# Performance work log

Hardware: AMD Instinct MI355X
Metric: run time of the kernel (lower is better)

The kernel has to match this reference:

```python
import jax, jax.numpy as jnp
import numpy as np

T = 1024
V = 512
K_BINS = jnp.array([1, 2, 3, 4, 5, 6, 7, 8, 12, 16, 24, 32, 48, 64, 96, 128], dtype=jnp.int32)
SPLIT_T = T // 2                      # int(T * 0.5)
CW = max(4, T // 20)                  # crossfade width = 51
FADE_START = SPLIT_T - CW // 2        # 487
FADE_END = SPLIT_T + CW // 2          # 537


def _early_weight():
    t = jnp.arange(T, dtype=jnp.float32)
    fade = 1.0 - (t - FADE_START) / (FADE_END - FADE_START)
    ew = jnp.where(t < FADE_START, 1.0, jnp.where(t < FADE_END, fade, 0.0))
    return ew.reshape(1, T, 1)


def setup_inputs() -> dict:
    key = jax.random.key(0)
    k = jax.random.split(key, 5)
    B = 64
    return {
        "x": jax.random.normal(k[0], (B, T, V), dtype=jnp.float32),
        "g_early_real": jax.random.normal(k[1], (V, 16), dtype=jnp.float32) * 0.1,
        "g_early_imag": jax.random.normal(k[2], (V, 16), dtype=jnp.float32) * 0.1,
        "g_late_real": jax.random.normal(k[3], (V, 16), dtype=jnp.float32) * 0.1,
        "g_late_imag": jax.random.normal(k[4], (V, 16), dtype=jnp.float32) * 0.1,
    }


def reference(x, g_early_real, g_early_imag, g_late_real, g_late_imag):
    # x: [B, T, V] real. rfft along time.
    X = jnp.fft.rfft(x, n=T, axis=1)              # [B, F, V] complex, F = T//2+1
    xb = X[:, K_BINS, :]                          # [B, K, V]
    # complex gain (1 + gr + i*gi), broadcast [1, K, V]
    g_e = (g_early_real + 1j * g_early_imag).T[None, :, :]
    g_l = (g_late_real + 1j * g_late_imag).T[None, :, :]
    Y_e = X.at[:, K_BINS, :].set(xb * (1.0 + g_e))
    Y_l = X.at[:, K_BINS, :].set(xb * (1.0 + g_l))
    y_early = jnp.fft.irfft(Y_e, n=T, axis=1)     # [B, T, V]
    y_late = jnp.fft.irfft(Y_l, n=T, axis=1)
    ew = _early_weight()
    return ew * y_early + (1.0 - ew) * y_late
```

## Files before the change

kernel.cpp:

```cpp
#include <hip/hip_runtime.h>
#include <math.h>

#define T_LEN 1024
#define VV 512
#define BB 64
#define NB 16
#define ANG_STEP 0.006135923151542565f
#define FADE_S 487
#define FADE_E 537

typedef float v2f __attribute__((ext_vector_type(2)));

__device__ constexpr int KB[NB] = {1,2,3,4,5,6,7,8,12,16,24,32,48,64,96,128};
__device__ constexpr float CWT[NB] = {
    0.9999811753f, 0.9999247018f, 0.9998305818f, 0.9996988187f,
    0.9995294175f, 0.9993223846f, 0.9990777278f, 0.9987954562f,
    0.9972904567f, 0.9951847267f, 0.9891765100f, 0.9807852804f,
    0.9569403357f, 0.9238795325f, 0.8314696123f, 0.7071067812f};
__device__ constexpr float SWT[NB] = {
    0.0061358846f, 0.0122715383f, 0.0184067299f, 0.0245412285f,
    0.0306748032f, 0.0368072229f, 0.0429382569f, 0.0490676743f,
    0.0735645636f, 0.0980171403f, 0.1467304745f, 0.1950903220f,
    0.2902846773f, 0.3826834324f, 0.5555702330f, 0.7071067812f};

__global__ __launch_bounds__(512) void k_fused(const float* __restrict__ x,
                                               const float* __restrict__ ger,
                                               const float* __restrict__ gei,
                                               const float* __restrict__ glr,
                                               const float* __restrict__ gli,
                                               float* __restrict__ Hg,
                                               float* __restrict__ out) {
    const int b    = blockIdx.x;
    const int vc   = blockIdx.y;
    const int tid  = threadIdx.x;
    const int wave = tid >> 6;
    const int lane = tid & 63;

    __shared__ __align__(16) float scr[4 * 128 * 8];

    const int trow = wave * 128;
    const int v0   = lane * 2;
    const float2* xrd = (const float2*)(x + ((size_t)b * T_LEN + trow) * VV + vc * 128) + lane;

    float ar0[NB], ai0[NB], ar1[NB], ai1[NB], c[NB], s[NB];
#pragma unroll
    for (int j = 0; j < NB; ++j) {
        ar0[j] = ai0[j] = ar1[j] = ai1[j] = 0.f;
        int n0 = (KB[j] * trow) & (T_LEN - 1);
        sincosf(ANG_STEP * (float)n0, &s[j], &c[j]);
    }

#define DFT_STEP(AV)                                            \
    do {                                                        \
        _Pragma("unroll")                                       \
        for (int j = 0; j < NB; ++j) {                          \
            ar0[j] = fmaf((AV).x, c[j], ar0[j]);                \
            ai0[j] = fmaf(-(AV).x, s[j], ai0[j]);               \
            ar1[j] = fmaf((AV).y, c[j], ar1[j]);                \
            ai1[j] = fmaf(-(AV).y, s[j], ai1[j]);               \
            float cn = fmaf(c[j], CWT[j], -(s[j] * SWT[j]));    \
            float sn = fmaf(s[j], CWT[j], c[j] * SWT[j]);       \
            c[j] = cn; s[j] = sn;                               \
        }                                                       \
    } while (0)

    {
        float2 a0 = xrd[(size_t)0 * 256];
        float2 a1 = xrd[(size_t)1 * 256];
        float2 a2 = xrd[(size_t)2 * 256];
        float2 a3 = xrd[(size_t)3 * 256];
#pragma unroll 1
        for (int i = 0; i < 124; i += 4) {
            float2 b0 = xrd[(size_t)(i + 4) * 256];
            float2 b1 = xrd[(size_t)(i + 5) * 256];
            float2 b2 = xrd[(size_t)(i + 6) * 256];
            float2 b3 = xrd[(size_t)(i + 7) * 256];
            DFT_STEP(a0); DFT_STEP(a1); DFT_STEP(a2); DFT_STEP(a3);
            a0 = b0; a1 = b1; a2 = b2; a3 = b3;
        }
        DFT_STEP(a0); DFT_STEP(a1); DFT_STEP(a2); DFT_STEP(a3);
    }
#undef DFT_STEP

    float Xre_lo[2], Xre_hi[2], Xim_lo[2], Xim_hi[2];

#define RED_ROUND(SRC0, SRC1, JOFF, DST)                                   \
    do {                                                                   \
        if (wave < 4) {                                                    \
            _Pragma("unroll")                                              \
            for (int jj = 0; jj < 8; ++jj) {                               \
                scr[((size_t)wave * 128 + v0)     * 8 + jj] = SRC0[(JOFF) + jj]; \
                scr[((size_t)wave * 128 + v0 + 1) * 8 + jj] = SRC1[(JOFF) + jj]; \
            }                                                              \
        }                                                                  \
        __syncthreads();                                                   \
        if (wave >= 4) {                                                   \
            const int w2 = wave - 4;                                       \
            _Pragma("unroll")                                              \
            for (int jj = 0; jj < 8; ++jj) {                               \
                scr[((size_t)w2 * 128 + v0)     * 8 + jj] += SRC0[(JOFF) + jj]; \
                scr[((size_t)w2 * 128 + v0 + 1) * 8 + jj] += SRC1[(JOFF) + jj]; \
            }                                                              \
        }                                                                  \
        __syncthreads();                                                   \
        _Pragma("unroll")                                                  \
        for (int q = 0; q < 2; ++q) {                                      \
            const int cc = tid * 2 + q;                                    \
            const int vq = cc >> 3, jq = cc & 7;                           \
            DST[q] = scr[((size_t)0 * 128 + vq) * 8 + jq]                  \
                   + scr[((size_t)1 * 128 + vq) * 8 + jq]                  \
                   + scr[((size_t)2 * 128 + vq) * 8 + jq]                  \
                   + scr[((size_t)3 * 128 + vq) * 8 + jq];                 \
        }                                                                  \
        __syncthreads();                                                   \
    } while (0)

    RED_ROUND(ar0, ar1, 0, Xre_lo);
    RED_ROUND(ar0, ar1, 8, Xre_hi);
    RED_ROUND(ai0, ai1, 0, Xim_lo);
    RED_ROUND(ai0, ai1, 8, Xim_hi);
#undef RED_ROUND

    const float scale = 2.0f / (float)T_LEN;
    {
        float* hg = Hg + (size_t)b * 64 * VV;
#pragma unroll
        for (int q = 0; q < 2; ++q) {
            const int cc = tid * 2 + q;
            const int vq = cc >> 3;
            const int vg = vc * 128 + vq;
#pragma unroll
            for (int half = 0; half < 2; ++half) {
                const int jq = (cc & 7) + half * 8;
                const float Xr = half ? Xre_hi[q] : Xre_lo[q];
                const float Xi = half ? Xim_hi[q] : Xim_lo[q];
                float er = ger[vg * NB + jq], ei = gei[vg * NB + jq];
                float lr = glr[vg * NB + jq], li = gli[vg * NB + jq];
                float here  = (Xr * er - Xi * ei) * scale;
                float heimN = -(Xr * ei + Xi * er) * scale;
                float hlre  = (Xr * lr - Xi * li) * scale;
                float hlimN = -(Xr * li + Xi * lr) * scale;
                hg[(size_t)jq * VV + vg]        = here;
                hg[(size_t)(16 + jq) * VV + vg] = heimN;
                hg[(size_t)(32 + jq) * VV + vg] = hlre;
                hg[(size_t)(48 + jq) * VV + vg] = hlimN;
            }
        }
    }
    __syncthreads();

    float hr0[NB], hi0[NB], hr1[NB], hi1[NB];
    {
        const int qb = (wave < 4) ? 0 : 32;
        const float* hgr = Hg + (size_t)b * 64 * VV + vc * 128;
#pragma unroll
        for (int j = 0; j < NB; ++j) {
            hr0[j] = hgr[(size_t)(qb + j) * VV + v0];
            hr1[j] = hgr[(size_t)(qb + j) * VV + v0 + 1];
            hi0[j] = hgr[(size_t)(qb + 16 + j) * VV + v0];
            hi1[j] = hgr[(size_t)(qb + 16 + j) * VV + v0 + 1];
        }
#pragma unroll
        for (int j = 0; j < NB; ++j) {
            int n0 = (KB[j] * trow) & (T_LEN - 1);
            sincosf(ANG_STEP * (float)n0, &s[j], &c[j]);
        }
    }

    v2f* ow = (v2f*)(out + ((size_t)b * T_LEN + trow) * VV + vc * 128) + lane;

#define APPLY_STEP(TT, AV)                                      \
    do {                                                        \
        float s0 = 0.f, s1 = 0.f;                               \
        _Pragma("unroll")                                       \
        for (int j = 0; j < NB; ++j) {                          \
            s0 = fmaf(hr0[j], c[j], s0);                        \
            s0 = fmaf(hi0[j], s[j], s0);                        \
            s1 = fmaf(hr1[j], c[j], s1);                        \
            s1 = fmaf(hi1[j], s[j], s1);                        \
            float cn = fmaf(c[j], CWT[j], -(s[j] * SWT[j]));    \
            float sn = fmaf(s[j], CWT[j], c[j] * SWT[j]);       \
            c[j] = cn; s[j] = sn;                               \
        }                                                       \
        v2f ov; ov.x = (AV).x + s0; ov.y = (AV).y + s1;         \
        __builtin_nontemporal_store(ov, &ow[(size_t)(TT) * 256]); \
    } while (0)

    {
        float2 a0 = xrd[(size_t)0 * 256];
        float2 a1 = xrd[(size_t)1 * 256];
        float2 a2 = xrd[(size_t)2 * 256];
        float2 a3 = xrd[(size_t)3 * 256];
#pragma unroll 1
        for (int i = 0; i < 124; i += 4) {
            float2 b0 = xrd[(size_t)(i + 4) * 256];
            float2 b1 = xrd[(size_t)(i + 5) * 256];
            float2 b2 = xrd[(size_t)(i + 6) * 256];
            float2 b3 = xrd[(size_t)(i + 7) * 256];
            APPLY_STEP(i + 0, a0); APPLY_STEP(i + 1, a1);
            APPLY_STEP(i + 2, a2); APPLY_STEP(i + 3, a3);
            a0 = b0; a1 = b1; a2 = b2; a3 = b3;
        }
        APPLY_STEP(124, a0); APPLY_STEP(125, a1);
        APPLY_STEP(126, a2); APPLY_STEP(127, a3);
    }
#undef APPLY_STEP
}

__global__ __launch_bounds__(512) void k_fixup(const float* __restrict__ x,
                                               const float* __restrict__ H,
                                               float* __restrict__ out) {
    const int b   = blockIdx.x;
    const int tz  = blockIdx.y;
    const int tid = threadIdx.x;
    const int ts  = tz ? 512 : FADE_S;
    const int te  = tz ? FADE_E : 512;
    const int nt  = te - ts;

    __shared__ float2 tab[32][NB];
    for (int i = tid; i < nt * NB; i += 512) {
        int t = i >> 4, j = i & 15;
        int idx = (KB[j] * (ts + t)) & (T_LEN - 1);
        float ss, cc; sincosf(ANG_STEP * (float)idx, &ss, &cc);
        tab[t][j] = make_float2(cc, ss);
    }

    float er[NB], ei[NB], lr[NB], li[NB];
    const float* hp = H + (size_t)b * 64 * VV + tid;
#pragma unroll
    for (int j = 0; j < NB; ++j) {
        er[j] = hp[(size_t)j        * VV];
        ei[j] = hp[(size_t)(16 + j) * VV];
        lr[j] = hp[(size_t)(32 + j) * VV];
        li[j] = hp[(size_t)(48 + j) * VV];
    }
    __syncthreads();

    const float* xrd = x + ((size_t)b * T_LEN + ts) * VV + tid;
    float*       ow  = out + ((size_t)b * T_LEN + ts) * VV + tid;

    for (int t = 0; t < nt; ++t) {
        float av = xrd[(size_t)t * VV];
        const int tg = ts + t;
        float se = 0.f, sl = 0.f;
#pragma unroll
        for (int j = 0; j < NB; ++j) {
            float2 cs = tab[t][j];
            se = fmaf(er[j], cs.x, se); se = fmaf(ei[j], cs.y, se);
            sl = fmaf(lr[j], cs.x, sl); sl = fmaf(li[j], cs.y, sl);
        }
        float w = 1.0f - (float)(tg - FADE_S) * (1.0f / 50.0f);
        ow[(size_t)t * VV] = av + fmaf(w, se - sl, sl);
    }
}

extern "C" void kernel_launch(void* const* d_in, const int* in_sizes, int n_in,
                              void* d_out, int out_size, void* d_ws, size_t ws_size,
                              hipStream_t stream) {
    (void)in_sizes; (void)n_in; (void)out_size; (void)ws_size;
    const float* x   = (const float*)d_in[0];
    const float* ger = (const float*)d_in[1];
    const float* gei = (const float*)d_in[2];
    const float* glr = (const float*)d_in[3];
    const float* gli = (const float*)d_in[4];
    float* out = (float*)d_out;

    float* Hg = (float*)d_ws;

    k_fused<<<dim3(BB, 4), 512, 0, stream>>>(x, ger, gei, glr, gli, Hg, out);
    k_fixup<<<dim3(BB, 2), 512, 0, stream>>>(x, Hg, out);
}
```

Baseline: 126.2 us.

## Double block size to 1024 threads, halve time rows per wave, stage gains in LDS

New measurement: 193.3 us. 1.53x slower.

```diff
diff --git a/kernel.cpp b/kernel.cpp
--- a/kernel.cpp
+++ b/kernel.cpp
@@ -23,22 +23,23 @@
     0.0735645636f, 0.0980171403f, 0.1467304745f, 0.1950903220f,
     0.2902846773f, 0.3826834324f, 0.5555702330f, 0.7071067812f};
 
-__global__ __launch_bounds__(512) void k_fused(const float* __restrict__ x,
-                                               const float* __restrict__ ger,
-                                               const float* __restrict__ gei,
-                                               const float* __restrict__ glr,
-                                               const float* __restrict__ gli,
-                                               float* __restrict__ Hg,
-                                               float* __restrict__ out) {
+__global__ __launch_bounds__(1024) void k_fused(const float* __restrict__ x,
+                                                const float* __restrict__ ger,
+                                                const float* __restrict__ gei,
+                                                const float* __restrict__ glr,
+                                                const float* __restrict__ gli,
+                                                float* __restrict__ Hg,
+                                                float* __restrict__ out) {
     const int b    = blockIdx.x;
     const int vc   = blockIdx.y;
     const int tid  = threadIdx.x;
     const int wave = tid >> 6;
     const int lane = tid & 63;
 
-    __shared__ __align__(16) float scr[4 * 128 * 8];
-
-    const int trow = wave * 128;
+    __shared__ __align__(16) float scr[8 * 128 * 9];
+    __shared__ __align__(16) float HB[64 * 128];
+
+    const int trow = wave * 64;
     const int v0   = lane * 2;
     const float2* xrd = (const float2*)(x + ((size_t)b * T_LEN + trow) * VV + vc * 128) + lane;
 
@@ -70,7 +71,7 @@
         float2 a2 = xrd[(size_t)2 * 256];
         float2 a3 = xrd[(size_t)3 * 256];
 #pragma unroll 1
-        for (int i = 0; i < 124; i += 4) {
+        for (int i = 0; i < 60; i += 4) {
             float2 b0 = xrd[(size_t)(i + 4) * 256];
             float2 b1 = xrd[(size_t)(i + 5) * 256];
             float2 b2 = xrd[(size_t)(i + 6) * 256];
@@ -82,37 +83,37 @@
     }
 #undef DFT_STEP
 
-    float Xre_lo[2], Xre_hi[2], Xim_lo[2], Xim_hi[2];
-
-#define RED_ROUND(SRC0, SRC1, JOFF, DST)                                   \
-    do {                                                                   \
-        if (wave < 4) {                                                    \
-            _Pragma("unroll")                                              \
-            for (int jj = 0; jj < 8; ++jj) {                               \
-                scr[((size_t)wave * 128 + v0)     * 8 + jj] = SRC0[(JOFF) + jj]; \
-                scr[((size_t)wave * 128 + v0 + 1) * 8 + jj] = SRC1[(JOFF) + jj]; \
-            }                                                              \
-        }                                                                  \
-        __syncthreads();                                                   \
-        if (wave >= 4) {                                                   \
-            const int w2 = wave - 4;                                       \
-            _Pragma("unroll")                                              \
-            for (int jj = 0; jj < 8; ++jj) {                               \
-                scr[((size_t)w2 * 128 + v0)     * 8 + jj] += SRC0[(JOFF) + jj]; \
-                scr[((size_t)w2 * 128 + v0 + 1) * 8 + jj] += SRC1[(JOFF) + jj]; \
-            }                                                              \
-        }                                                                  \
-        __syncthreads();                                                   \
-        _Pragma("unroll")                                                  \
-        for (int q = 0; q < 2; ++q) {                                      \
-            const int cc = tid * 2 + q;                                    \
-            const int vq = cc >> 3, jq = cc & 7;                           \
-            DST[q] = scr[((size_t)0 * 128 + vq) * 8 + jq]                  \
-                   + scr[((size_t)1 * 128 + vq) * 8 + jq]                  \
-                   + scr[((size_t)2 * 128 + vq) * 8 + jq]                  \
-                   + scr[((size_t)3 * 128 + vq) * 8 + jq];                 \
-        }                                                                  \
-        __syncthreads();                                                   \
+    float Xre_lo, Xre_hi, Xim_lo, Xim_hi;
+    const int vq = tid >> 3;
+    const int jq = tid & 7;
+
+#define RED_ROUND(SRC0, SRC1, JOFF, DST)                                         \
+    do {                                                                         \
+        if (wave < 8) {                                                          \
+            _Pragma("unroll")                                                    \
+            for (int jj = 0; jj < 8; ++jj) {                                     \
+                scr[((size_t)wave * 128 + v0)     * 9 + jj] = SRC0[(JOFF) + jj]; \
+                scr[((size_t)wave * 128 + v0 + 1) * 9 + jj] = SRC1[(JOFF) + jj]; \
+            }                                                                    \
+        }                                                                        \
+        __syncthreads();                                                         \
+        if (wave >= 8) {                                                         \
+            const int w2 = wave - 8;                                             \
+            _Pragma("unroll")                                                    \
+            for (int jj = 0; jj < 8; ++jj) {                                     \
+                scr[((size_t)w2 * 128 + v0)     * 9 + jj] += SRC0[(JOFF) + jj];  \
+                scr[((size_t)w2 * 128 + v0 + 1) * 9 + jj] += SRC1[(JOFF) + jj];  \
+            }                                                                    \
+        }                                                                        \
+        __syncthreads();                                                         \
+        {                                                                        \
+            float acc = 0.f;                                                     \
+            _Pragma("unroll")                                                    \
+            for (int w = 0; w < 8; ++w)                                          \
+                acc += scr[((size_t)w * 128 + vq) * 9 + jq];                     \
+            DST = acc;                                                           \
+        }                                                                        \
+        __syncthreads();                                                         \
     } while (0)
 
     RED_ROUND(ar0, ar1, 0, Xre_lo);
@@ -124,41 +125,39 @@
     const float scale = 2.0f / (float)T_LEN;
     {
         float* hg = Hg + (size_t)b * 64 * VV;
-#pragma unroll
-        for (int q = 0; q < 2; ++q) {
-            const int cc = tid * 2 + q;
-            const int vq = cc >> 3;
-            const int vg = vc * 128 + vq;
-#pragma unroll
-            for (int half = 0; half < 2; ++half) {
-                const int jq = (cc & 7) + half * 8;
-                const float Xr = half ? Xre_hi[q] : Xre_lo[q];
-                const float Xi = half ? Xim_hi[q] : Xim_lo[q];
-                float er = ger[vg * NB + jq], ei = gei[vg * NB + jq];
-                float lr = glr[vg * NB + jq], li = gli[vg * NB + jq];
-                float here  = (Xr * er - Xi * ei) * scale;
-                float heimN = -(Xr * ei + Xi * er) * scale;
-                float hlre  = (Xr * lr - Xi * li) * scale;
-                float hlimN = -(Xr * li + Xi * lr) * scale;
-                hg[(size_t)jq * VV + vg]        = here;
-                hg[(size_t)(16 + jq) * VV + vg] = heimN;
-                hg[(size_t)(32 + jq) * VV + vg] = hlre;
-                hg[(size_t)(48 + jq) * VV + vg] = hlimN;
-            }
+        const int vg = vc * 128 + vq;
+#pragma unroll
+        for (int half = 0; half < 2; ++half) {
+            const int jc = jq + half * 8;
+            const float Xr = half ? Xre_hi : Xre_lo;
+            const float Xi = half ? Xim_hi : Xim_lo;
+            float er = ger[vg * NB + jc], ei = gei[vg * NB + jc];
+            float lr = glr[vg * NB + jc], li = gli[vg * NB + jc];
+            float here  = (Xr * er - Xi * ei) * scale;
+            float heimN = -(Xr * ei + Xi * er) * scale;
+            float hlre  = (Xr * lr - Xi * li) * scale;
+            float hlimN = -(Xr * li + Xi * lr) * scale;
+            HB[jc * 128 + vq]        = here;
+            HB[(16 + jc) * 128 + vq] = heimN;
+            HB[(32 + jc) * 128 + vq] = hlre;
+            HB[(48 + jc) * 128 + vq] = hlimN;
+            hg[(size_t)jc * VV + vg]        = here;
+            hg[(size_t)(16 + jc) * VV + vg] = heimN;
+            hg[(size_t)(32 + jc) * VV + vg] = hlre;
+            hg[(size_t)(48 + jc) * VV + vg] = hlimN;
         }
     }
     __syncthreads();
 
     float hr0[NB], hi0[NB], hr1[NB], hi1[NB];
     {
-        const int qb = (wave < 4) ? 0 : 32;
-        const float* hgr = Hg + (size_t)b * 64 * VV + vc * 128;
+        const int qb = (wave < 8) ? 0 : 32;
 #pragma unroll
         for (int j = 0; j < NB; ++j) {
-            hr0[j] = hgr[(size_t)(qb + j) * VV + v0];
-            hr1[j] = hgr[(size_t)(qb + j) * VV + v0 + 1];
-            hi0[j] = hgr[(size_t)(qb + 16 + j) * VV + v0];
-            hi1[j] = hgr[(size_t)(qb + 16 + j) * VV + v0 + 1];
+            hr0[j] = HB[(qb + j) * 128 + v0];
+            hr1[j] = HB[(qb + j) * 128 + v0 + 1];
+            hi0[j] = HB[(qb + 16 + j) * 128 + v0];
+            hi1[j] = HB[(qb + 16 + j) * 128 + v0 + 1];
         }
 #pragma unroll
         for (int j = 0; j < NB; ++j) {
@@ -192,7 +191,7 @@
         float2 a2 = xrd[(size_t)2 * 256];
         float2 a3 = xrd[(size_t)3 * 256];
 #pragma unroll 1
-        for (int i = 0; i < 124; i += 4) {
+        for (int i = 0; i < 60; i += 4) {
             float2 b0 = xrd[(size_t)(i + 4) * 256];
             float2 b1 = xrd[(size_t)(i + 5) * 256];
             float2 b2 = xrd[(size_t)(i + 6) * 256];
@@ -201,8 +200,8 @@
             APPLY_STEP(i + 2, a2); APPLY_STEP(i + 3, a3);
             a0 = b0; a1 = b1; a2 = b2; a3 = b3;
         }
-        APPLY_STEP(124, a0); APPLY_STEP(125, a1);
-        APPLY_STEP(126, a2); APPLY_STEP(127, a3);
+        APPLY_STEP(60, a0); APPLY_STEP(61, a1);
+        APPLY_STEP(62, a2); APPLY_STEP(63, a3);
     }
 #undef APPLY_STEP
 }
@@ -267,6 +266,6 @@
 
     float* Hg = (float*)d_ws;
 
-    k_fused<<<dim3(BB, 4), 512, 0, stream>>>(x, ger, gei, glr, gli, Hg, out);
+    k_fused<<<dim3(BB, 4), 1024, 0, stream>>>(x, ger, gei, glr, gli, Hg, out);
     k_fixup<<<dim3(BB, 2), 512, 0, stream>>>(x, Hg, out);
 }
```

## Halve per-thread columns, doubling grid, and use Chebyshev twiddle recurrence

Applied to the files above, without the earlier changes.

Result: slower. 131.9 us (+4.5%).

```diff
diff --git a/kernel.cpp b/kernel.cpp
--- a/kernel.cpp
+++ b/kernel.cpp
@@ -8,8 +8,6 @@
 #define ANG_STEP 0.006135923151542565f
 #define FADE_S 487
 #define FADE_E 537
-
-typedef float v2f __attribute__((ext_vector_type(2)));
 
 __device__ constexpr int KB[NB] = {1,2,3,4,5,6,7,8,12,16,24,32,48,64,96,128};
 __device__ constexpr float CWT[NB] = {
@@ -22,6 +20,11 @@
     0.0306748032f, 0.0368072229f, 0.0429382569f, 0.0490676743f,
     0.0735645636f, 0.0980171403f, 0.1467304745f, 0.1950903220f,
     0.2902846773f, 0.3826834324f, 0.5555702330f, 0.7071067812f};
+__device__ constexpr float C2W[NB] = {
+    1.9999623506f, 1.9998494036f, 1.9996611636f, 1.9993976374f,
+    1.9990588350f, 1.9986447692f, 1.9981554556f, 1.9975909124f,
+    1.9945809134f, 1.9903694534f, 1.9783530200f, 1.9615705608f,
+    1.9138806714f, 1.8477590650f, 1.6629392246f, 1.4142135624f};
 
 __global__ __launch_bounds__(512) void k_fused(const float* __restrict__ x,
                                                const float* __restrict__ ger,
@@ -36,45 +39,45 @@
     const int wave = tid >> 6;
     const int lane = tid & 63;
 
-    __shared__ __align__(16) float scr[4 * 128 * 8];
+    __shared__ __align__(16) float scr[4 * 64 * 17];
+    __shared__ __align__(16) float HB[64 * 64];
 
     const int trow = wave * 128;
-    const int v0   = lane * 2;
-    const float2* xrd = (const float2*)(x + ((size_t)b * T_LEN + trow) * VV + vc * 128) + lane;
-
-    float ar0[NB], ai0[NB], ar1[NB], ai1[NB], c[NB], s[NB];
+    const float* xrd = x + ((size_t)b * T_LEN + trow) * VV + vc * 64 + lane;
+
+    float ar[NB], ai[NB], c[NB], s[NB], cp[NB], sp[NB];
 #pragma unroll
     for (int j = 0; j < NB; ++j) {
-        ar0[j] = ai0[j] = ar1[j] = ai1[j] = 0.f;
+        ar[j] = ai[j] = 0.f;
         int n0 = (KB[j] * trow) & (T_LEN - 1);
         sincosf(ANG_STEP * (float)n0, &s[j], &c[j]);
-    }
-
-#define DFT_STEP(AV)                                            \
-    do {                                                        \
-        _Pragma("unroll")                                       \
-        for (int j = 0; j < NB; ++j) {                          \
-            ar0[j] = fmaf((AV).x, c[j], ar0[j]);                \
-            ai0[j] = fmaf(-(AV).x, s[j], ai0[j]);               \
-            ar1[j] = fmaf((AV).y, c[j], ar1[j]);                \
-            ai1[j] = fmaf(-(AV).y, s[j], ai1[j]);               \
-            float cn = fmaf(c[j], CWT[j], -(s[j] * SWT[j]));    \
-            float sn = fmaf(s[j], CWT[j], c[j] * SWT[j]);       \
-            c[j] = cn; s[j] = sn;                               \
-        }                                                       \
+        cp[j] = fmaf(c[j], CWT[j], s[j] * SWT[j]);
+        sp[j] = fmaf(s[j], CWT[j], -(c[j] * SWT[j]));
+    }
+
+#define DFT_STEP(AV)                                           \
+    do {                                                       \
+        _Pragma("unroll")                                      \
+        for (int j = 0; j < NB; ++j) {                         \
+            ar[j] = fmaf((AV), c[j], ar[j]);                   \
+            ai[j] = fmaf(-(AV), s[j], ai[j]);                  \
+            float cn = fmaf(C2W[j], c[j], -cp[j]);             \
+            float sn = fmaf(C2W[j], s[j], -sp[j]);             \
+            cp[j] = c[j]; sp[j] = s[j]; c[j] = cn; s[j] = sn;  \
+        }                                                      \
     } while (0)
 
     {
-        float2 a0 = xrd[(size_t)0 * 256];
-        float2 a1 = xrd[(size_t)1 * 256];
-        float2 a2 = xrd[(size_t)2 * 256];
-        float2 a3 = xrd[(size_t)3 * 256];
+        float a0 = xrd[(size_t)0 * VV];
+        float a1 = xrd[(size_t)1 * VV];
+        float a2 = xrd[(size_t)2 * VV];
+        float a3 = xrd[(size_t)3 * VV];
 #pragma unroll 1
         for (int i = 0; i < 124; i += 4) {
-            float2 b0 = xrd[(size_t)(i + 4) * 256];
-            float2 b1 = xrd[(size_t)(i + 5) * 256];
-            float2 b2 = xrd[(size_t)(i + 6) * 256];
-            float2 b3 = xrd[(size_t)(i + 7) * 256];
+            float b0 = xrd[(size_t)(i + 4) * VV];
+            float b1 = xrd[(size_t)(i + 5) * VV];
+            float b2 = xrd[(size_t)(i + 6) * VV];
+            float b3 = xrd[(size_t)(i + 7) * VV];
             DFT_STEP(a0); DFT_STEP(a1); DFT_STEP(a2); DFT_STEP(a3);
             a0 = b0; a1 = b1; a2 = b2; a3 = b3;
         }
@@ -82,44 +85,54 @@
     }
 #undef DFT_STEP
 
-    float Xre_lo[2], Xre_hi[2], Xim_lo[2], Xim_hi[2];
-
-#define RED_ROUND(SRC0, SRC1, JOFF, DST)                                   \
-    do {                                                                   \
-        if (wave < 4) {                                                    \
-            _Pragma("unroll")                                              \
-            for (int jj = 0; jj < 8; ++jj) {                               \
-                scr[((size_t)wave * 128 + v0)     * 8 + jj] = SRC0[(JOFF) + jj]; \
-                scr[((size_t)wave * 128 + v0 + 1) * 8 + jj] = SRC1[(JOFF) + jj]; \
-            }                                                              \
-        }                                                                  \
-        __syncthreads();                                                   \
-        if (wave >= 4) {                                                   \
-            const int w2 = wave - 4;                                       \
-            _Pragma("unroll")                                              \
-            for (int jj = 0; jj < 8; ++jj) {                               \
-                scr[((size_t)w2 * 128 + v0)     * 8 + jj] += SRC0[(JOFF) + jj]; \
-                scr[((size_t)w2 * 128 + v0 + 1) * 8 + jj] += SRC1[(JOFF) + jj]; \
-            }                                                              \
-        }                                                                  \
-        __syncthreads();                                                   \
-        _Pragma("unroll")                                                  \
-        for (int q = 0; q < 2; ++q) {                                      \
-            const int cc = tid * 2 + q;                                    \
-            const int vq = cc >> 3, jq = cc & 7;                           \
-            DST[q] = scr[((size_t)0 * 128 + vq) * 8 + jq]                  \
-                   + scr[((size_t)1 * 128 + vq) * 8 + jq]                  \
-                   + scr[((size_t)2 * 128 + vq) * 8 + jq]                  \
-                   + scr[((size_t)3 * 128 + vq) * 8 + jq];                 \
-        }                                                                  \
-        __syncthreads();                                                   \
-    } while (0)
-
-    RED_ROUND(ar0, ar1, 0, Xre_lo);
-    RED_ROUND(ar0, ar1, 8, Xre_hi);
-    RED_ROUND(ai0, ai1, 0, Xim_lo);
-    RED_ROUND(ai0, ai1, 8, Xim_hi);
-#undef RED_ROUND
+    float Xre[2], Xim[2];
+
+    if (wave < 4) {
+#pragma unroll
+        for (int j = 0; j < NB; ++j)
+            scr[((size_t)wave * 64 + lane) * 17 + j] = ar[j];
+    }
+    __syncthreads();
+    if (wave >= 4) {
+        const int w2 = wave - 4;
+#pragma unroll
+        for (int j = 0; j < NB; ++j)
+            scr[((size_t)w2 * 64 + lane) * 17 + j] += ar[j];
+    }
+    __syncthreads();
+#pragma unroll
+    for (int q = 0; q < 2; ++q) {
+        const int cc = tid * 2 + q;
+        const int vq = cc >> 4, jq = cc & 15;
+        Xre[q] = scr[((size_t)0 * 64 + vq) * 17 + jq]
+               + scr[((size_t)1 * 64 + vq) * 17 + jq]
+               + scr[((size_t)2 * 64 + vq) * 17 + jq]
+               + scr[((size_t)3 * 64 + vq) * 17 + jq];
+    }
+    __syncthreads();
+
+    if (wave < 4) {
+#pragma unroll
+        for (int j = 0; j < NB; ++j)
+            scr[((size_t)wave * 64 + lane) * 17 + j] = ai[j];
+    }
+    __syncthreads();
+    if (wave >= 4) {
+        const int w2 = wave - 4;
+#pragma unroll
+        for (int j = 0; j < NB; ++j)
+            scr[((size_t)w2 * 64 + lane) * 17 + j] += ai[j];
+    }
+    __syncthreads();
+#pragma unroll
+    for (int q = 0; q < 2; ++q) {
+        const int cc = tid * 2 + q;
+        const int vq = cc >> 4, jq = cc & 15;
+        Xim[q] = scr[((size_t)0 * 64 + vq) * 17 + jq]
+               + scr[((size_t)1 * 64 + vq) * 17 + jq]
+               + scr[((size_t)2 * 64 + vq) * 17 + jq]
+               + scr[((size_t)3 * 64 + vq) * 17 + jq];
+    }
 
     const float scale = 2.0f / (float)T_LEN;
     {
@@ -127,76 +140,71 @@
 #pragma unroll
         for (int q = 0; q < 2; ++q) {
             const int cc = tid * 2 + q;
-            const int vq = cc >> 3;
-            const int vg = vc * 128 + vq;
-#pragma unroll
-            for (int half = 0; half < 2; ++half) {
-                const int jq = (cc & 7) + half * 8;
-                const float Xr = half ? Xre_hi[q] : Xre_lo[q];
-                const float Xi = half ? Xim_hi[q] : Xim_lo[q];
-                float er = ger[vg * NB + jq], ei = gei[vg * NB + jq];
-                float lr = glr[vg * NB + jq], li = gli[vg * NB + jq];
-                float here  = (Xr * er - Xi * ei) * scale;
-                float heimN = -(Xr * ei + Xi * er) * scale;
-                float hlre  = (Xr * lr - Xi * li) * scale;
-                float hlimN = -(Xr * li + Xi * lr) * scale;
-                hg[(size_t)jq * VV + vg]        = here;
-                hg[(size_t)(16 + jq) * VV + vg] = heimN;
-                hg[(size_t)(32 + jq) * VV + vg] = hlre;
-                hg[(size_t)(48 + jq) * VV + vg] = hlimN;
-            }
-        }
-    }
-    __syncthreads();
-
-    float hr0[NB], hi0[NB], hr1[NB], hi1[NB];
+            const int vq = cc >> 4, jq = cc & 15;
+            const int vg = vc * 64 + vq;
+            float er = ger[vg * NB + jq], ei = gei[vg * NB + jq];
+            float lr = glr[vg * NB + jq], li = gli[vg * NB + jq];
+            float here  = (Xre[q] * er - Xim[q] * ei) * scale;
+            float heimN = -(Xre[q] * ei + Xim[q] * er) * scale;
+            float hlre  = (Xre[q] * lr - Xim[q] * li) * scale;
+            float hlimN = -(Xre[q] * li + Xim[q] * lr) * scale;
+            HB[jq * 64 + vq]        = here;
+            HB[(16 + jq) * 64 + vq] = heimN;
+            HB[(32 + jq) * 64 + vq] = hlre;
+            HB[(48 + jq) * 64 + vq] = hlimN;
+            hg[(size_t)jq * VV + vg]        = here;
+            hg[(size_t)(16 + jq) * VV + vg] = heimN;
+            hg[(size_t)(32 + jq) * VV + vg] = hlre;
+            hg[(size_t)(48 + jq) * VV + vg] = hlimN;
+        }
+    }
+    __syncthreads();
+
+    float hr[NB], hi[NB];
     {
         const int qb = (wave < 4) ? 0 : 32;
-        const float* hgr = Hg + (size_t)b * 64 * VV + vc * 128;
 #pragma unroll
         for (int j = 0; j < NB; ++j) {
-            hr0[j] = hgr[(size_t)(qb + j) * VV + v0];
-            hr1[j] = hgr[(size_t)(qb + j) * VV + v0 + 1];
-            hi0[j] = hgr[(size_t)(qb + 16 + j) * VV + v0];
-            hi1[j] = hgr[(size_t)(qb + 16 + j) * VV + v0 + 1];
+            hr[j] = HB[(qb + j) * 64 + lane];
+            hi[j] = HB[(qb + 16 + j) * 64 + lane];
         }
 #pragma unroll
         for (int j = 0; j < NB; ++j) {
             int n0 = (KB[j] * trow) & (T_LEN - 1);
             sincosf(ANG_STEP * (float)n0, &s[j], &c[j]);
-        }
-    }
-
-    v2f* ow = (v2f*)(out + ((size_t)b * T_LEN + trow) * VV + vc * 128) + lane;
-
-#define APPLY_STEP(TT, AV)                                      \
-    do {                                                        \
-        float s0 = 0.f, s1 = 0.f;                               \
-        _Pragma("unroll")                                       \
-        for (int j = 0; j < NB; ++j) {                          \
-            s0 = fmaf(hr0[j], c[j], s0);                        \
-            s0 = fmaf(hi0[j], s[j], s0);                        \
-            s1 = fmaf(hr1[j], c[j], s1);                        \
-            s1 = fmaf(hi1[j], s[j], s1);                        \
-            float cn = fmaf(c[j], CWT[j], -(s[j] * SWT[j]));    \
-            float sn = fmaf(s[j], CWT[j], c[j] * SWT[j]);       \
-            c[j] = cn; s[j] = sn;                               \
-        }                                                       \
-        v2f ov; ov.x = (AV).x + s0; ov.y = (AV).y + s1;         \
-        __builtin_nontemporal_store(ov, &ow[(size_t)(TT) * 256]); \
+            cp[j] = fmaf(c[j], CWT[j], s[j] * SWT[j]);
+            sp[j] = fmaf(s[j], CWT[j], -(c[j] * SWT[j]));
+        }
+    }
+
+    float* ow = out + ((size_t)b * T_LEN + trow) * VV + vc * 64 + lane;
+
+#define APPLY_STEP(TT, AV)                                     \
+    do {                                                       \
+        float s0 = 0.f;                                        \
+        _Pragma("unroll")                                      \
+        for (int j = 0; j < NB; ++j) {                         \
+            s0 = fmaf(hr[j], c[j], s0);                        \
+            s0 = fmaf(hi[j], s[j], s0);                        \
+            float cn = fmaf(C2W[j], c[j], -cp[j]);             \
+            float sn = fmaf(C2W[j], s[j], -sp[j]);             \
+            cp[j] = c[j]; sp[j] = s[j]; c[j] = cn; s[j] = sn;  \
+        }                                                      \
+        __builtin_nontemporal_store((AV) + s0,                 \
+            &ow[(size_t)(TT) * VV]);                           \
     } while (0)
 
     {
-        float2 a0 = xrd[(size_t)0 * 256];
-        float2 a1 = xrd[(size_t)1 * 256];
-        float2 a2 = xrd[(size_t)2 * 256];
-        float2 a3 = xrd[(size_t)3 * 256];
+        float a0 = xrd[(size_t)0 * VV];
+        float a1 = xrd[(size_t)1 * VV];
+        float a2 = xrd[(size_t)2 * VV];
+        float a3 = xrd[(size_t)3 * VV];
 #pragma unroll 1
         for (int i = 0; i < 124; i += 4) {
-            float2 b0 = xrd[(size_t)(i + 4) * 256];
-            float2 b1 = xrd[(size_t)(i + 5) * 256];
-            float2 b2 = xrd[(size_t)(i + 6) * 256];
-            float2 b3 = xrd[(size_t)(i + 7) * 256];
+            float b0 = xrd[(size_t)(i + 4) * VV];
+            float b1 = xrd[(size_t)(i + 5) * VV];
+            float b2 = xrd[(size_t)(i + 6) * VV];
+            float b3 = xrd[(size_t)(i + 7) * VV];
             APPLY_STEP(i + 0, a0); APPLY_STEP(i + 1, a1);
             APPLY_STEP(i + 2, a2); APPLY_STEP(i + 3, a3);
             a0 = b0; a1 = b1; a2 = b2; a3 = b3;
@@ -267,6 +275,6 @@
 
     float* Hg = (float*)d_ws;
 
-    k_fused<<<dim3(BB, 4), 512, 0, stream>>>(x, ger, gei, glr, gli, Hg, out);
+    k_fused<<<dim3(BB, 8), 512, 0, stream>>>(x, ger, gei, glr, gli, Hg, out);
     k_fixup<<<dim3(BB, 2), 512, 0, stream>>>(x, Hg, out);
 }
```

## Split fused DFT/apply kernel into two kernels over time halves for more blocks

Applied to the files above, without the earlier changes.

New measurement: 129.0 us. 1.02x slower.

```diff
diff --git a/kernel.cpp b/kernel.cpp
--- a/kernel.cpp
+++ b/kernel.cpp
@@ -23,22 +23,18 @@
     0.0735645636f, 0.0980171403f, 0.1467304745f, 0.1950903220f,
     0.2902846773f, 0.3826834324f, 0.5555702330f, 0.7071067812f};
 
-__global__ __launch_bounds__(512) void k_fused(const float* __restrict__ x,
-                                               const float* __restrict__ ger,
-                                               const float* __restrict__ gei,
-                                               const float* __restrict__ glr,
-                                               const float* __restrict__ gli,
-                                               float* __restrict__ Hg,
-                                               float* __restrict__ out) {
+__global__ __launch_bounds__(512) void k_dft(const float* __restrict__ x,
+                                             float* __restrict__ Xpart) {
     const int b    = blockIdx.x;
     const int vc   = blockIdx.y;
+    const int th   = blockIdx.z;
     const int tid  = threadIdx.x;
     const int wave = tid >> 6;
     const int lane = tid & 63;
 
-    __shared__ __align__(16) float scr[4 * 128 * 8];
-
-    const int trow = wave * 128;
+    __shared__ __align__(16) float scr[4 * 128 * 17];
+
+    const int trow = th * 512 + wave * 64;
     const int v0   = lane * 2;
     const float2* xrd = (const float2*)(x + ((size_t)b * T_LEN + trow) * VV + vc * 128) + lane;
 
@@ -70,7 +66,7 @@
         float2 a2 = xrd[(size_t)2 * 256];
         float2 a3 = xrd[(size_t)3 * 256];
 #pragma unroll 1
-        for (int i = 0; i < 124; i += 4) {
+        for (int i = 0; i < 60; i += 4) {
             float2 b0 = xrd[(size_t)(i + 4) * 256];
             float2 b1 = xrd[(size_t)(i + 5) * 256];
             float2 b2 = xrd[(size_t)(i + 6) * 256];
@@ -82,91 +78,118 @@
     }
 #undef DFT_STEP
 
-    float Xre_lo[2], Xre_hi[2], Xim_lo[2], Xim_hi[2];
-
-#define RED_ROUND(SRC0, SRC1, JOFF, DST)                                   \
+    float Xre[4], Xim[4];
+
+#define RED_ROUND(SRC0, SRC1, DST)                                         \
     do {                                                                   \
         if (wave < 4) {                                                    \
             _Pragma("unroll")                                              \
-            for (int jj = 0; jj < 8; ++jj) {                               \
-                scr[((size_t)wave * 128 + v0)     * 8 + jj] = SRC0[(JOFF) + jj]; \
-                scr[((size_t)wave * 128 + v0 + 1) * 8 + jj] = SRC1[(JOFF) + jj]; \
+            for (int j = 0; j < NB; ++j) {                                 \
+                scr[((size_t)wave * 128 + v0)     * 17 + j] = SRC0[j];     \
+                scr[((size_t)wave * 128 + v0 + 1) * 17 + j] = SRC1[j];     \
             }                                                              \
         }                                                                  \
         __syncthreads();                                                   \
         if (wave >= 4) {                                                   \
             const int w2 = wave - 4;                                       \
             _Pragma("unroll")                                              \
-            for (int jj = 0; jj < 8; ++jj) {                               \
-                scr[((size_t)w2 * 128 + v0)     * 8 + jj] += SRC0[(JOFF) + jj]; \
-                scr[((size_t)w2 * 128 + v0 + 1) * 8 + jj] += SRC1[(JOFF) + jj]; \
+            for (int j = 0; j < NB; ++j) {                                 \
+                scr[((size_t)w2 * 128 + v0)     * 17 + j] += SRC0[j];      \
+                scr[((size_t)w2 * 128 + v0 + 1) * 17 + j] += SRC1[j];      \
             }                                                              \
         }                                                                  \
         __syncthreads();                                                   \
         _Pragma("unroll")                                                  \
-        for (int q = 0; q < 2; ++q) {                                      \
-            const int cc = tid * 2 + q;                                    \
-            const int vq = cc >> 3, jq = cc & 7;                           \
-            DST[q] = scr[((size_t)0 * 128 + vq) * 8 + jq]                  \
-                   + scr[((size_t)1 * 128 + vq) * 8 + jq]                  \
-                   + scr[((size_t)2 * 128 + vq) * 8 + jq]                  \
-                   + scr[((size_t)3 * 128 + vq) * 8 + jq];                 \
+        for (int q = 0; q < 4; ++q) {                                      \
+            const int cc = tid * 4 + q;                                    \
+            const int vq = cc >> 4, jq = cc & 15;                          \
+            DST[q] = scr[((size_t)0 * 128 + vq) * 17 + jq]                 \
+                   + scr[((size_t)1 * 128 + vq) * 17 + jq]                 \
+                   + scr[((size_t)2 * 128 + vq) * 17 + jq]                 \
+                   + scr[((size_t)3 * 128 + vq) * 17 + jq];                \
         }                                                                  \
         __syncthreads();                                                   \
     } while (0)
 
-    RED_ROUND(ar0, ar1, 0, Xre_lo);
-    RED_ROUND(ar0, ar1, 8, Xre_hi);
-    RED_ROUND(ai0, ai1, 0, Xim_lo);
-    RED_ROUND(ai0, ai1, 8, Xim_hi);
+    RED_ROUND(ar0, ar1, Xre);
+    RED_ROUND(ai0, ai1, Xim);
 #undef RED_ROUND
+
+    float* xp = Xpart + ((size_t)((b * 4 + vc) * 2 + th)) * 32 * 128;
+#pragma unroll
+    for (int q = 0; q < 4; ++q) {
+        const int cc = tid * 4 + q;
+        const int vq = cc >> 4, jq = cc & 15;
+        xp[(size_t)jq * 128 + vq]        = Xre[q];
+        xp[(size_t)(16 + jq) * 128 + vq] = Xim[q];
+    }
+}
+
+__global__ __launch_bounds__(512) void k_comb_apply(const float* __restrict__ x,
+                                                    const float* __restrict__ ger,
+                                                    const float* __restrict__ gei,
+                                                    const float* __restrict__ glr,
+                                                    const float* __restrict__ gli,
+                                                    const float* __restrict__ Xpart,
+                                                    float* __restrict__ Hg,
+                                                    float* __restrict__ out) {
+    const int b    = blockIdx.x;
+    const int vc   = blockIdx.y;
+    const int th   = blockIdx.z;
+    const int tid  = threadIdx.x;
+    const int wave = tid >> 6;
+    const int lane = tid & 63;
+
+    __shared__ __align__(16) float HB[64 * 128];
 
     const float scale = 2.0f / (float)T_LEN;
     {
+        const float* xp0 = Xpart + ((size_t)((b * 4 + vc) * 2 + 0)) * 32 * 128;
+        const float* xp1 = Xpart + ((size_t)((b * 4 + vc) * 2 + 1)) * 32 * 128;
         float* hg = Hg + (size_t)b * 64 * VV;
 #pragma unroll
-        for (int q = 0; q < 2; ++q) {
-            const int cc = tid * 2 + q;
-            const int vq = cc >> 3;
-            const int vg = vc * 128 + vq;
-#pragma unroll
-            for (int half = 0; half < 2; ++half) {
-                const int jq = (cc & 7) + half * 8;
-                const float Xr = half ? Xre_hi[q] : Xre_lo[q];
-                const float Xi = half ? Xim_hi[q] : Xim_lo[q];
-                float er = ger[vg * NB + jq], ei = gei[vg * NB + jq];
-                float lr = glr[vg * NB + jq], li = gli[vg * NB + jq];
-                float here  = (Xr * er - Xi * ei) * scale;
-                float heimN = -(Xr * ei + Xi * er) * scale;
-                float hlre  = (Xr * lr - Xi * li) * scale;
-                float hlimN = -(Xr * li + Xi * lr) * scale;
-                hg[(size_t)jq * VV + vg]        = here;
-                hg[(size_t)(16 + jq) * VV + vg] = heimN;
-                hg[(size_t)(32 + jq) * VV + vg] = hlre;
-                hg[(size_t)(48 + jq) * VV + vg] = hlimN;
+        for (int k = 0; k < 4; ++k) {
+            const int idx = tid + k * 512;
+            const int j = idx >> 7, v = idx & 127;
+            const int vg = vc * 128 + v;
+            float Xr = xp0[(size_t)j * 128 + v]        + xp1[(size_t)j * 128 + v];
+            float Xi = xp0[(size_t)(16 + j) * 128 + v] + xp1[(size_t)(16 + j) * 128 + v];
+            float er = ger[vg * NB + j], ei = gei[vg * NB + j];
+            float lr = glr[vg * NB + j], li = gli[vg * NB + j];
+            float here  = (Xr * er - Xi * ei) * scale;
+            float heimN = -(Xr * ei + Xi * er) * scale;
+            float hlre  = (Xr * lr - Xi * li) * scale;
+            float hlimN = -(Xr * li + Xi * lr) * scale;
+            HB[(size_t)j * 128 + v]        = here;
+            HB[(size_t)(16 + j) * 128 + v] = heimN;
+            HB[(size_t)(32 + j) * 128 + v] = hlre;
+            HB[(size_t)(48 + j) * 128 + v] = hlimN;
+            if (th == 0) {
+                hg[(size_t)j * VV + vg]        = here;
+                hg[(size_t)(16 + j) * VV + vg] = heimN;
+                hg[(size_t)(32 + j) * VV + vg] = hlre;
+                hg[(size_t)(48 + j) * VV + vg] = hlimN;
             }
         }
     }
     __syncthreads();
 
-    float hr0[NB], hi0[NB], hr1[NB], hi1[NB];
-    {
-        const int qb = (wave < 4) ? 0 : 32;
-        const float* hgr = Hg + (size_t)b * 64 * VV + vc * 128;
-#pragma unroll
-        for (int j = 0; j < NB; ++j) {
-            hr0[j] = hgr[(size_t)(qb + j) * VV + v0];
-            hr1[j] = hgr[(size_t)(qb + j) * VV + v0 + 1];
-            hi0[j] = hgr[(size_t)(qb + 16 + j) * VV + v0];
-            hi1[j] = hgr[(size_t)(qb + 16 + j) * VV + v0 + 1];
-        }
-#pragma unroll
-        for (int j = 0; j < NB; ++j) {
-            int n0 = (KB[j] * trow) & (T_LEN - 1);
-            sincosf(ANG_STEP * (float)n0, &s[j], &c[j]);
-        }
-    }
-
+    const int trow = th * 512 + wave * 64;
+    const int v0   = lane * 2;
+    const int qb   = th ? 32 : 0;
+
+    float hr0[NB], hi0[NB], hr1[NB], hi1[NB], c[NB], s[NB];
+#pragma unroll
+    for (int j = 0; j < NB; ++j) {
+        hr0[j] = HB[(size_t)(qb + j) * 128 + v0];
+        hr1[j] = HB[(size_t)(qb + j) * 128 + v0 + 1];
+        hi0[j] = HB[(size_t)(qb + 16 + j) * 128 + v0];
+        hi1[j] = HB[(size_t)(qb + 16 + j) * 128 + v0 + 1];
+        int n0 = (KB[j] * trow) & (T_LEN - 1);
+        sincosf(ANG_STEP * (float)n0, &s[j], &c[j]);
+    }
+
+    const float2* xrd = (const float2*)(x + ((size_t)b * T_LEN + trow) * VV + vc * 128) + lane;
     v2f* ow = (v2f*)(out + ((size_t)b * T_LEN + trow) * VV + vc * 128) + lane;
 
 #define APPLY_STEP(TT, AV)                                      \
@@ -192,7 +215,7 @@
         float2 a2 = xrd[(size_t)2 * 256];
         float2 a3 = xrd[(size_t)3 * 256];
 #pragma unroll 1
-        for (int i = 0; i < 124; i += 4) {
+        for (int i = 0; i < 60; i += 4) {
             float2 b0 = xrd[(size_t)(i + 4) * 256];
             float2 b1 = xrd[(size_t)(i + 5) * 256];
             float2 b2 = xrd[(size_t)(i + 6) * 256];
@@ -201,8 +224,8 @@
             APPLY_STEP(i + 2, a2); APPLY_STEP(i + 3, a3);
             a0 = b0; a1 = b1; a2 = b2; a3 = b3;
         }
-        APPLY_STEP(124, a0); APPLY_STEP(125, a1);
-        APPLY_STEP(126, a2); APPLY_STEP(127, a3);
+        APPLY_STEP(60, a0); APPLY_STEP(61, a1);
+        APPLY_STEP(62, a2); APPLY_STEP(63, a3);
     }
 #undef APPLY_STEP
 }
@@ -265,8 +288,10 @@
     const float* gli = (const float*)d_in[4];
     float* out = (float*)d_out;
 
-    float* Hg = (float*)d_ws;
-
-    k_fused<<<dim3(BB, 4), 512, 0, stream>>>(x, ger, gei, glr, gli, Hg, out);
+    float* Hg    = (float*)d_ws;
+    float* Xpart = Hg + (size_t)BB * 64 * VV;
+
+    k_dft<<<dim3(BB, 4, 2), 512, 0, stream>>>(x, Xpart);
+    k_comb_apply<<<dim3(BB, 4, 2), 512, 0, stream>>>(x, ger, gei, glr, gli, Xpart, Hg, out);
     k_fixup<<<dim3(BB, 2), 512, 0, stream>>>(x, Hg, out);
 }
```
